# Optimization experiments

Hardware: AMD Instinct MI355X
Metric: run time of the kernel (lower is better)

The kernel has to match this reference:

```python
import jax, jax.numpy as jnp
import numpy as np

EPS = 1e-12  # matches F.normalize default eps

def _l2_normalize(x, axis=-1):
    n = jnp.sqrt(jnp.sum(x * x, axis=axis, keepdims=True))
    return x / jnp.maximum(n, EPS)

def setup_inputs() -> dict:
    key = jax.random.key(0)
    k1, k2, k3 = jax.random.split(key, 3)
    B, C, D, V = 1024, 262144, 512, 512
    query = jax.random.normal(k1, (B, D), dtype=jnp.float32)
    keys = jax.random.normal(k2, (C, D), dtype=jnp.float32)
    values = jax.random.normal(k3, (C, V), dtype=jnp.float32)
    return {"query": query, "keys": keys, "values": values, "k": 8}

def reference(query, keys, values, k):
    # Cosine similarity: normalize both sides, then GEMM.
    q_norm = _l2_normalize(query, axis=1)          # [B, D]
    k_norm = _l2_normalize(keys, axis=1)           # [C, D]
    scores = jnp.matmul(q_norm, k_norm.T)          # [B, C]
    top_scores, top_indices = jax.lax.top_k(scores, k)  # [B, k] each
    # Vectorized gather replacing the per-row Python loop:
    retrieved_values = values[top_indices]         # [B, k, V]
    return retrieved_values, top_scores, top_indices
```

## Files before the change

kernel.cpp:

```cpp
#include <hip/hip_runtime.h>
#include <hip/hip_bf16.h>
#include <stdint.h>

#define B_Q   1024
#define C_K   262144
#define D_DIM 512
#define V_DIM 512
#define K_TOP 8
#define BM 128
#define BN 128
#define NT (C_K/BN)
#define NKT 8
#define TPB 32
#define CAP 2048
#define QS 8.0f
#define TAU_S 8.64f
#define RWIN 64
#define SC1 0x7F7F7F7F

typedef float f32x4  __attribute__((ext_vector_type(4)));
typedef float f32x16 __attribute__((ext_vector_type(16)));
typedef int   i32x8  __attribute__((ext_vector_type(8)));
typedef __attribute__((address_space(3))) unsigned char lds_uchar;
typedef __attribute__((address_space(1))) const unsigned char gbl_uchar;

__global__ __launch_bounds__(256) void pack_rows(const float* __restrict__ in,
                                                 uint8_t* __restrict__ outp,
                                                 int nrows, int* cnt, int ncnt){
  if (cnt != nullptr && blockIdx.x == 0){
    for (int i = threadIdx.x; i < ncnt; i += 256) cnt[i] = 0;
  }
  int row  = blockIdx.x*4 + (threadIdx.x>>6);
  int lane = threadIdx.x & 63;
  if (row >= nrows) return;
  const float4* r4 = (const float4*)(in + (size_t)row*D_DIM);
  float4 a = r4[lane*2], b = r4[lane*2+1];
  float ss = a.x*a.x+a.y*a.y+a.z*a.z+a.w*a.w
           + b.x*b.x+b.y*b.y+b.z*b.z+b.w*b.w;
  #pragma unroll
  for (int off=32; off>0; off>>=1) ss += __shfl_xor(ss, off);
  float rn = QS / fmaxf(sqrtf(ss), 1e-12f);
  int w0 = __builtin_amdgcn_cvt_pk_fp8_f32(a.x*rn, a.y*rn, 0,  false);
  w0     = __builtin_amdgcn_cvt_pk_fp8_f32(a.z*rn, a.w*rn, w0, true);
  int w1 = __builtin_amdgcn_cvt_pk_fp8_f32(b.x*rn, b.y*rn, 0,  false);
  w1     = __builtin_amdgcn_cvt_pk_fp8_f32(b.z*rn, b.w*rn, w1, true);
  const int j  = lane;
  const int rt = row >> 5, rr = row & 31;
  const int kt = j >> 3, h = (j >> 2) & 1, sub = (j >> 1) & 1;
  uint2* dst = (uint2*)(outp + ((size_t)(rt*8 + kt))*2048
                        + sub*1024 + (rr + 32*h)*16 + (j & 1)*8);
  *dst = make_uint2((unsigned)w0, (unsigned)w1);
}

__global__ __launch_bounds__(512) void gemm_topk(const uint8_t* __restrict__ qp,
                                                 const uint8_t* __restrict__ kp,
                                                 int* __restrict__ cnt,
                                                 float2* __restrict__ cand){
  extern __shared__ __align__(16) unsigned char alds[];

  const int tid  = threadIdx.x;
  const int lane = tid & 63;
  const int w    = tid >> 6;
  const int wm = w >> 2, wn = w & 3;

  const unsigned bid = blockIdx.x;
  const int xcd  = bid & 7;
  const int s    = bid >> 3;
  const int mt   = s & 7;
  const int nt0  = xcd*256 + (s >> 3)*TPB;

  #pragma unroll
  for (int i=0; i<8; i++)
    __builtin_amdgcn_global_load_lds(
        (gbl_uchar*)(qp + (size_t)mt*65536u + tid*16 + i*8192),
        (lds_uchar*)(alds + tid*16 + i*8192), 16, 0, 0);
  __syncthreads();

  f32x16 acc0 = {0}, acc1 = {0};
  union frag8 { uint4 q[2]; i32x8 v; };

  const uint8_t* bptr = kp + ((size_t)(nt0*4 + wn)*8)*2048 + (unsigned)lane*16u;
  uint4 pf0 = *(const uint4*)(bptr);
  uint4 pf1 = *(const uint4*)(bptr + 1024);

  const unsigned aoffA = (unsigned)(wm*16)*2048u + (unsigned)lane*16u;

  #define EPILOG(accR_, mh_) do{                                                \
    const int rbase = mt*BM + wm*64 + (mh_)*32 + 4*(lane>>5);                    \
    _Pragma("unroll")                                                            \
    for (int qd=0; qd<4; qd++){                                                  \
      float v0=(accR_)[qd*4+0], v1=(accR_)[qd*4+1];                              \
      float v2=(accR_)[qd*4+2], v3=(accR_)[qd*4+3];                              \
      float mx = fmaxf(fmaxf(v0,v1), fmaxf(v2,v3));                              \
      if (mx > TAU_S){                                                           \
        _Pragma("unroll")                                                        \
        for (int jj=0; jj<4; jj++){                                              \
          float v = (accR_)[qd*4+jj];                                            \
          if (v > TAU_S){                                                        \
            int rowg = rbase + jj + 8*qd;                                        \
            int pos = atomicAdd(cnt + rowg, 1);                                  \
            if (pos < CAP)                                                       \
              cand[(size_t)rowg*CAP + pos] = make_float2(v, __int_as_float(colg)); \
          }                                                                      \
        }                                                                        \
      }                                                                          \
    }                                                                            \
  }while(0)

  for (int t=0; t<TPB; t++){
    #pragma unroll
    for (int k8=0; k8<8; k8++){
      const bool last = (t == TPB-1) && (k8 == 7);
      const uint8_t* bnext = bptr + (k8 == 7 ? 25*2048 : 2048);
      uint4 nf0, nf1;
      if (!last){
        nf0 = *(const uint4*)(bnext);
        nf1 = *(const uint4*)(bnext + 1024);
      }
      frag8 fa0, fa1, fb;
      const unsigned ao = aoffA + (unsigned)k8*2048u;
      fa0.q[0] = *(const uint4*)(alds + ao);
      fa0.q[1] = *(const uint4*)(alds + ao + 1024u);
      fa1.q[0] = *(const uint4*)(alds + ao + 16384u);
      fa1.q[1] = *(const uint4*)(alds + ao + 16384u + 1024u);
      fb.q[0] = pf0; fb.q[1] = pf1;
      __builtin_amdgcn_s_setprio(1);
      acc0 = __builtin_amdgcn_mfma_scale_f32_32x32x64_f8f6f4(
                 fa0.v, fb.v, acc0, 0, 0, 0, SC1, 0, SC1);
      acc1 = __builtin_amdgcn_mfma_scale_f32_32x32x64_f8f6f4(
                 fa1.v, fb.v, acc1, 0, 0, 0, SC1, 0, SC1);
      __builtin_amdgcn_s_setprio(0);
      pf0 = nf0; pf1 = nf1;
      bptr = bnext;
    }

    {
      const int ntc  = nt0 + t;
      const int colg = ntc*BN + wn*32 + (lane&31);
      EPILOG(acc0, 0);
      EPILOG(acc1, 1);
      acc0 = (f32x16){0}; acc1 = (f32x16){0};
    }
  }
  #undef EPILOG
}

__global__ __launch_bounds__(256) void merge_rescore(const int* __restrict__ cnt,
                                                     const float2* __restrict__ cand,
                                                     const float* __restrict__ q,
                                                     const float* __restrict__ keys,
                                                     const float* __restrict__ values,
                                                     float* __restrict__ out){
  const int qi = blockIdx.x, tid = threadIdx.x;
  const int lane = tid & 63, w = tid >> 6;
  __shared__ __align__(16) float qrow[D_DIM];
  __shared__ __align__(16) float2 ent[CAP];
  __shared__ int    widx[RWIN];
  __shared__ double dsc[RWIN];
  __shared__ double wq[4];
  __shared__ int    fidx[8];
  __shared__ double fsc[8];

  float2 qv = ((const float2*)(q + (size_t)qi*D_DIM))[tid];
  qrow[tid*2] = qv.x; qrow[tid*2+1] = qv.y;
  double pq = (double)qv.x*qv.x + (double)qv.y*qv.y;
  #pragma unroll
  for (int off=32; off>0; off>>=1) pq += __shfl_xor(pq, off);
  if (lane == 0) wq[w] = pq;

  const int n = min(cnt[qi], CAP);
  for (int i = tid; i < n; i += 256) ent[i] = cand[(size_t)qi*CAP + i];
  if (tid < RWIN) widx[tid] = -1;
  __syncthreads();
  double qq = wq[0]+wq[1]+wq[2]+wq[3];

  for (int e = tid; e < n; e += 256){
    float se = ent[e].x; int ce = __float_as_int(ent[e].y);
    int rank = 0;
    for (int jx = 0; jx < n; jx++){
      float sj = ent[jx].x; int cj = __float_as_int(ent[jx].y);
      rank += (sj > se) || (sj == se && cj < ce);
    }
    if (rank < RWIN) widx[rank] = ce;
  }
  __syncthreads();

  const int g = tid >> 2, sub = tid & 3;
  const int ki = widx[g];
  const int kis = (ki < 0) ? 0 : ki;
  const float4* kr4 = (const float4*)(keys + (size_t)kis*D_DIM);
  const float4* qr4 = (const float4*)qrow;
  double da = 0.0, dk = 0.0;
  for (int i=0;i<32;i++){
    float4 kv  = kr4[sub*32+i];
    float4 qv4 = qr4[sub*32+i];
    da += (double)qv4.x*kv.x + (double)qv4.y*kv.y + (double)qv4.z*kv.z + (double)qv4.w*kv.w;
    dk += (double)kv.x*kv.x + (double)kv.y*kv.y + (double)kv.z*kv.z + (double)kv.w*kv.w;
  }
  da += __shfl_down(da, 2, 4); da += __shfl_down(da, 1, 4);
  dk += __shfl_down(dk, 2, 4); dk += __shfl_down(dk, 1, 4);
  if (sub == 0){
    double nq = fmax(sqrt(qq), 1e-12);
    double nk = fmax(sqrt(dk), 1e-12);
    dsc[g] = (ki < 0) ? -1e300 : da/(nq*nk);
  }
  __syncthreads();

  if (tid == 0){
    for (int s=0; s<8; s++){
      double bs = -1e301; int bi = 0; int bx = 0x7fffffff;
      for (int c=0; c<RWIN; c++){
        double v = dsc[c]; int ix = widx[c];
        if (v > bs || (v == bs && ix >= 0 && ix < bx)){ bs = v; bi = c; bx = ix; }
      }
      fsc[s] = bs; fidx[s] = (bx == 0x7fffffff) ? 0 : bx;
      dsc[bi] = -1e302;
    }
  }
  __syncthreads();

  float* out_sc  = out + (size_t)B_Q*K_TOP*V_DIM;
  float* out_idx = out_sc + (size_t)B_Q*K_TOP;
  if (tid < 8){
    out_sc [qi*K_TOP + tid] = (float)fsc[tid];
    out_idx[qi*K_TOP + tid] = (float)fidx[tid];
  }
  #pragma unroll
  for (int s=0; s<8; s++){
    const float2* vr = (const float2*)(values + (size_t)fidx[s]*V_DIM);
    float2* orow = (float2*)(out + ((size_t)qi*K_TOP + s)*V_DIM);
    orow[tid] = vr[tid];
  }
}

extern "C" void kernel_launch(void* const* d_in, const int* in_sizes, int n_in,
                              void* d_out, int out_size, void* d_ws, size_t ws_size,
                              hipStream_t stream){
  const float* q      = (const float*)d_in[0];
  const float* keys   = (const float*)d_in[1];
  const float* values = (const float*)d_in[2];
  unsigned char* ws = (unsigned char*)d_ws;
  uint8_t* qp = (uint8_t*)ws;
  uint8_t* kp = qp + (size_t)B_Q*D_DIM;
  int*    cnt  = (int*)(ws + (size_t)(B_Q + C_K)*D_DIM);
  float2* cand = (float2*)(ws + (size_t)(B_Q + C_K)*D_DIM + 8192);
  float* out = (float*)d_out;

  hipFuncSetAttribute((const void*)gemm_topk,
                      hipFuncAttributeMaxDynamicSharedMemorySize, 65536);

  pack_rows<<<dim3(B_Q/4), dim3(256), 0, stream>>>(q, qp, B_Q, cnt, B_Q);
  pack_rows<<<dim3(C_K/4), dim3(256), 0, stream>>>(keys, kp, C_K, nullptr, 0);
  gemm_topk<<<dim3(512), dim3(512), 65536, stream>>>(qp, kp, cnt, cand);
  merge_rescore<<<dim3(B_Q), dim3(256), 0, stream>>>(cnt, cand, q, keys, values, out);
}
```

Measured before the change: 451.9 us.

## Stage packed fp8 rows in LDS for coalesced stores; deepen B prefetch

The pack kernel now handles a 32-row tile per block. Each row is split over 8 threads, the fp8 fragments are written into an LDS staging buffer in MFMA layout, and the tile is then copied out with fully coalesced 16-byte stores instead of scattered 8-byte writes. Separately, the GEMM main loop is flattened into a single step loop with a three-deep register prefetch of key fragments, so global load latency has more time to hide. The costs are more register pressure and a redundant reload at the tail, and each pack thread now reads its source row twice.

```diff
diff --git a/kernel.cpp b/kernel.cpp
--- a/kernel.cpp
+++ b/kernel.cpp
@@ -10,7 +10,6 @@
 #define BM 128
 #define BN 128
 #define NT (C_K/BN)
-#define NKT 8
 #define TPB 32
 #define CAP 2048
 #define QS 8.0f
@@ -26,30 +25,43 @@
 
 __global__ __launch_bounds__(256) void pack_rows(const float* __restrict__ in,
                                                  uint8_t* __restrict__ outp,
-                                                 int nrows, int* cnt, int ncnt){
+                                                 int* cnt, int ncnt){
   if (cnt != nullptr && blockIdx.x == 0){
     for (int i = threadIdx.x; i < ncnt; i += 256) cnt[i] = 0;
   }
-  int row  = blockIdx.x*4 + (threadIdx.x>>6);
-  int lane = threadIdx.x & 63;
-  if (row >= nrows) return;
-  const float4* r4 = (const float4*)(in + (size_t)row*D_DIM);
-  float4 a = r4[lane*2], b = r4[lane*2+1];
-  float ss = a.x*a.x+a.y*a.y+a.z*a.z+a.w*a.w
-           + b.x*b.x+b.y*b.y+b.z*b.z+b.w*b.w;
-  #pragma unroll
-  for (int off=32; off>0; off>>=1) ss += __shfl_xor(ss, off);
-  float rn = QS / fmaxf(sqrtf(ss), 1e-12f);
-  int w0 = __builtin_amdgcn_cvt_pk_fp8_f32(a.x*rn, a.y*rn, 0,  false);
-  w0     = __builtin_amdgcn_cvt_pk_fp8_f32(a.z*rn, a.w*rn, w0, true);
-  int w1 = __builtin_amdgcn_cvt_pk_fp8_f32(b.x*rn, b.y*rn, 0,  false);
-  w1     = __builtin_amdgcn_cvt_pk_fp8_f32(b.z*rn, b.w*rn, w1, true);
-  const int j  = lane;
-  const int rt = row >> 5, rr = row & 31;
-  const int kt = j >> 3, h = (j >> 2) & 1, sub = (j >> 1) & 1;
-  uint2* dst = (uint2*)(outp + ((size_t)(rt*8 + kt))*2048
-                        + sub*1024 + (rr + 32*h)*16 + (j & 1)*8);
-  *dst = make_uint2((unsigned)w0, (unsigned)w1);
+  __shared__ __align__(16) unsigned char stg[16384];
+  const int tid = threadIdx.x;
+  const int r = tid >> 3;
+  const int c = tid & 7;
+  const int rt = blockIdx.x;
+  const size_t row = (size_t)rt*32 + r;
+  const float4* src = (const float4*)(in + row*D_DIM + c*64);
+
+  float ss = 0.f;
+  #pragma unroll
+  for (int i=0;i<16;i++){
+    float4 x = src[i];
+    ss += x.x*x.x + x.y*x.y + x.z*x.z + x.w*x.w;
+  }
+  ss += __shfl_xor(ss, 1); ss += __shfl_xor(ss, 2); ss += __shfl_xor(ss, 4);
+  const float rn = QS / fmaxf(sqrtf(ss), 1e-12f);
+
+  #pragma unroll
+  for (int jl=0; jl<8; jl++){
+    float4 a = src[jl*2], b = src[jl*2+1];
+    int w0 = __builtin_amdgcn_cvt_pk_fp8_f32(a.x*rn, a.y*rn, 0,  false);
+    w0     = __builtin_amdgcn_cvt_pk_fp8_f32(a.z*rn, a.w*rn, w0, true);
+    int w1 = __builtin_amdgcn_cvt_pk_fp8_f32(b.x*rn, b.y*rn, 0,  false);
+    w1     = __builtin_amdgcn_cvt_pk_fp8_f32(b.z*rn, b.w*rn, w1, true);
+    unsigned off = (unsigned)c*2048u + ((jl>>1)&1)*1024u
+                 + (unsigned)(r + 32*((jl>>2)&1))*16u + (jl&1)*8u;
+    *(uint2*)(stg + off) = make_uint2((unsigned)w0, (unsigned)w1);
+  }
+  __syncthreads();
+  uint4* g = (uint4*)(outp + (size_t)rt*16384u);
+  const uint4* s4 = (const uint4*)stg;
+  #pragma unroll
+  for (int p=0; p<4; p++) g[tid + p*256] = s4[tid + p*256];
 }
 
 __global__ __launch_bounds__(512) void gemm_topk(const uint8_t* __restrict__ qp,
@@ -79,9 +91,12 @@
   f32x16 acc0 = {0}, acc1 = {0};
   union frag8 { uint4 q[2]; i32x8 v; };
 
-  const uint8_t* bptr = kp + ((size_t)(nt0*4 + wn)*8)*2048 + (unsigned)lane*16u;
-  uint4 pf0 = *(const uint4*)(bptr);
-  uint4 pf1 = *(const uint4*)(bptr + 1024);
+  const uint8_t* bb = kp + ((size_t)(nt0*4 + wn)*8)*2048 + (unsigned)lane*16u;
+  #define BADDR(s_) (bb + (size_t)((s_)>>3)*65536u + (unsigned)(((s_)&7)*2048u))
+
+  uint4 b0a = *(const uint4*)(BADDR(0)), b0b = *(const uint4*)(BADDR(0)+1024);
+  uint4 b1a = *(const uint4*)(BADDR(1)), b1b = *(const uint4*)(BADDR(1)+1024);
+  uint4 b2a = *(const uint4*)(BADDR(2)), b2b = *(const uint4*)(BADDR(2)+1024);
 
   const unsigned aoffA = (unsigned)(wm*16)*2048u + (unsigned)lane*16u;
 
@@ -107,35 +122,29 @@
     }                                                                            \
   }while(0)
 
-  for (int t=0; t<TPB; t++){
-    #pragma unroll
-    for (int k8=0; k8<8; k8++){
-      const bool last = (t == TPB-1) && (k8 == 7);
-      const uint8_t* bnext = bptr + (k8 == 7 ? 25*2048 : 2048);
-      uint4 nf0, nf1;
-      if (!last){
-        nf0 = *(const uint4*)(bnext);
-        nf1 = *(const uint4*)(bnext + 1024);
-      }
-      frag8 fa0, fa1, fb;
-      const unsigned ao = aoffA + (unsigned)k8*2048u;
-      fa0.q[0] = *(const uint4*)(alds + ao);
-      fa0.q[1] = *(const uint4*)(alds + ao + 1024u);
-      fa1.q[0] = *(const uint4*)(alds + ao + 16384u);
-      fa1.q[1] = *(const uint4*)(alds + ao + 16384u + 1024u);
-      fb.q[0] = pf0; fb.q[1] = pf1;
-      __builtin_amdgcn_s_setprio(1);
-      acc0 = __builtin_amdgcn_mfma_scale_f32_32x32x64_f8f6f4(
-                 fa0.v, fb.v, acc0, 0, 0, 0, SC1, 0, SC1);
-      acc1 = __builtin_amdgcn_mfma_scale_f32_32x32x64_f8f6f4(
-                 fa1.v, fb.v, acc1, 0, 0, 0, SC1, 0, SC1);
-      __builtin_amdgcn_s_setprio(0);
-      pf0 = nf0; pf1 = nf1;
-      bptr = bnext;
-    }
-
-    {
-      const int ntc  = nt0 + t;
+  #pragma unroll 8
+  for (int st=0; st<TPB*8; st++){
+    frag8 fa0, fa1, fb;
+    const unsigned ao = aoffA + (unsigned)(st&7)*2048u;
+    fa0.q[0] = *(const uint4*)(alds + ao);
+    fa0.q[1] = *(const uint4*)(alds + ao + 1024u);
+    fa1.q[0] = *(const uint4*)(alds + ao + 16384u);
+    fa1.q[1] = *(const uint4*)(alds + ao + 16384u + 1024u);
+    fb.q[0] = b0a; fb.q[1] = b0b;
+    __builtin_amdgcn_s_setprio(1);
+    acc0 = __builtin_amdgcn_mfma_scale_f32_32x32x64_f8f6f4(
+               fa0.v, fb.v, acc0, 0, 0, 0, SC1, 0, SC1);
+    acc1 = __builtin_amdgcn_mfma_scale_f32_32x32x64_f8f6f4(
+               fa1.v, fb.v, acc1, 0, 0, 0, SC1, 0, SC1);
+    __builtin_amdgcn_s_setprio(0);
+    b0a = b1a; b0b = b1b;
+    b1a = b2a; b1b = b2b;
+    const int sn = (st+3 < TPB*8) ? st+3 : TPB*8-1;
+    b2a = *(const uint4*)(BADDR(sn));
+    b2b = *(const uint4*)(BADDR(sn) + 1024);
+
+    if ((st&7) == 7){
+      const int ntc  = nt0 + (st>>3);
       const int colg = ntc*BN + wn*32 + (lane&31);
       EPILOG(acc0, 0);
       EPILOG(acc1, 1);
@@ -143,6 +152,7 @@
     }
   }
   #undef EPILOG
+  #undef BADDR
 }
 
 __global__ __launch_bounds__(256) void merge_rescore(const int* __restrict__ cnt,
@@ -249,8 +259,8 @@
   hipFuncSetAttribute((const void*)gemm_topk,
                       hipFuncAttributeMaxDynamicSharedMemorySize, 65536);
 
-  pack_rows<<<dim3(B_Q/4), dim3(256), 0, stream>>>(q, qp, B_Q, cnt, B_Q);
-  pack_rows<<<dim3(C_K/4), dim3(256), 0, stream>>>(keys, kp, C_K, nullptr, 0);
+  pack_rows<<<dim3(B_Q/32), dim3(256), 0, stream>>>(q, qp, cnt, B_Q);
+  pack_rows<<<dim3(C_K/32), dim3(256), 0, stream>>>(keys, kp, nullptr, 0);
   gemm_topk<<<dim3(512), dim3(512), 65536, stream>>>(qp, kp, cnt, cand);
   merge_rescore<<<dim3(B_Q), dim3(256), 0, stream>>>(cnt, cand, q, keys, values, out);
 }
```

Measured after the change: 534.0 us. 1.18x slower.
